# Kernel optimization log

Hardware: AMD Instinct MI355X
Metric: run time of the kernel (lower is better)

Reference implementation:

```python
import jax, jax.numpy as jnp
import numpy as np

B, N, D, H, ADIM = 2048, 8, 128, 512, 6  # batch, n_slots, slot_dim, latent_dim, action_dim
EPS = 1e-5

# static fully-connected edge list (no self-loops), C-SWM convention: row=source (also receiver)
_adj = np.ones((N, N)) - np.eye(N)
_ROW, _COL = np.nonzero(_adj)
ROW = jnp.asarray(_ROW)
COL = jnp.asarray(_COL)
E = N * (N - 1)


def _layernorm(x, g, b):
    m = jnp.mean(x, axis=-1, keepdims=True)
    v = jnp.var(x, axis=-1, keepdims=True)
    return (x - m) * jax.lax.rsqrt(v + EPS) * g + b


def setup_inputs() -> dict:
    key = jax.random.key(0)
    ks = jax.random.split(key, 16)
    s = 0.02
    inp = {
        "slots": jax.random.normal(ks[0], (B, N, D), dtype=jnp.float32),
        # edge MLP: Linear(2D,H) ReLU Linear(H,H) LN ReLU Linear(H,H)
        "ew1": jax.random.normal(ks[1], (H, 2 * D), dtype=jnp.float32) * s,
        "eb1": jnp.zeros((H,), jnp.float32),
        "ew2": jax.random.normal(ks[2], (H, H), dtype=jnp.float32) * s,
        "eb2": jnp.zeros((H,), jnp.float32),
        "eln_g": jnp.ones((H,), jnp.float32),
        "eln_b": jnp.zeros((H,), jnp.float32),
        "ew3": jax.random.normal(ks[3], (H, H), dtype=jnp.float32) * s,
        "eb3": jnp.zeros((H,), jnp.float32),
        # node MLP: Linear(D+H,H) ReLU Linear(H,H) LN ReLU Linear(H,D)
        "nw1": jax.random.normal(ks[4], (H, D + H), dtype=jnp.float32) * s,
        "nb1": jnp.zeros((H,), jnp.float32),
        "nw2": jax.random.normal(ks[5], (H, H), dtype=jnp.float32) * s,
        "nb2": jnp.zeros((H,), jnp.float32),
        "nln_g": jnp.ones((H,), jnp.float32),
        "nln_b": jnp.zeros((H,), jnp.float32),
        "nw3": jax.random.normal(ks[6], (D, H), dtype=jnp.float32) * s,
        "nb3": jnp.zeros((D,), jnp.float32),
        # policy head: Linear(D, 2*action_dim)
        "head_w": jax.random.normal(ks[7], (2 * ADIM, D), dtype=jnp.float32) * s,
        "head_b": jnp.zeros((2 * ADIM,), jnp.float32),
    }
    return inp


def reference(slots, ew1, eb1, ew2, eb2, eln_g, eln_b, ew3, eb3,
              nw1, nb1, nw2, nb2, nln_g, nln_b, nw3, nb3, head_w, head_b):
    # ---- GNN edge model over all ordered pairs (i != j) ----
    src = slots[:, ROW]          # [B, E, D]
    tgt = slots[:, COL]          # [B, E, D]
    e = jnp.concatenate([src, tgt], axis=-1)            # [B, E, 2D]
    e = jax.nn.relu(jnp.einsum('bed,hd->beh', e, ew1) + eb1)
    e = jnp.einsum('beh,gh->beg', e, ew2) + eb2
    e = jax.nn.relu(_layernorm(e, eln_g, eln_b))
    e = jnp.einsum('beh,gh->beg', e, ew3) + eb3         # [B, E, H]
    # scatter-sum messages to source node index (unsorted_segment_sum over ROW)
    agg = jnp.zeros((slots.shape[0], N, e.shape[-1]), e.dtype).at[:, ROW].add(e)
    # ---- node model ----
    x = jnp.concatenate([slots, agg], axis=-1)          # [B, N, D+H]
    x = jax.nn.relu(jnp.einsum('bnd,hd->bnh', x, nw1) + nb1)
    x = jnp.einsum('bnh,gh->bng', x, nw2) + nb2
    x = jax.nn.relu(_layernorm(x, nln_g, nln_b))
    x = jnp.einsum('bnh,dh->bnd', x, nw3) + nb3         # [B, N, D]
    # ---- OCPolicy: ReLU, sum-pool over slots, linear head ----
    x = jax.nn.relu(x)
    pooled = x.sum(axis=1)                              # [B, D]
    return pooled @ head_w.T + head_b                   # [B, 2*ADIM]
```

## Files before the change

### kernel.cpp

```cpp
#include <hip/hip_runtime.h>
#include <cstdint>
#include <cstddef>

typedef _Float16 f16;
typedef _Float16 f16x8 __attribute__((ext_vector_type(8)));
typedef _Float16 f16x4 __attribute__((ext_vector_type(4)));
typedef float f32x4 __attribute__((ext_vector_type(4)));

#define AS1 __attribute__((address_space(1)))
#define AS3 __attribute__((address_space(3)))

__device__ __forceinline__ void gl_lds16(const void* g, void* l) {
    __builtin_amdgcn_global_load_lds((const AS1 uint32_t*)g, (AS3 uint32_t*)l, 16, 0, 0);
}

__device__ __forceinline__ f16x8 relu8(f16x8 x) {
    f16x8 z = {};
    return __builtin_elementwise_max(x, z);
}


__global__ __launch_bounds__(256, 2)
void edge_gemm_fused(const f16* __restrict__ PQ, const f16* __restrict__ W,
                     const float* __restrict__ bias, f16* __restrict__ C)
{
    __shared__ f16 Bs[2][8192];
    __shared__ f16 PQl[2][2048];
    const int tid  = threadIdx.x;
    const int wave = tid >> 6, lane = tid & 63;
    const int wm = wave >> 1, wn = wave & 1;
    const int lr = lane & 15, lk = lane >> 4;
    const int row0 = blockIdx.y << 7;
    const int col0 = blockIdx.x << 8;

    const int sc16 = (((tid & 3) ^ ((tid >> 3) & 3)) << 3);
    const f16* Wg = W + (size_t)(col0 + (tid >> 2)) * 512 + sc16;
    const int b0 = row0 / 56;
    const int n0 = b0 << 3;
    const f16* PQg = PQ + (size_t)(n0 + ((tid & 127) >> 2)) * 1024
                   + ((tid >> 7) << 9) + sc16;

    int addrP[4], addrQ[4];
#pragma unroll
    for (int i = 0; i < 4; ++i) {
        int row = wm * 64 + i * 16 + lr;
        int er  = row0 + row;
        int bb  = er / 56;
        int e   = er - bb * 56;
        int r   = e / 7;
        int t2  = e - r * 7;
        int cn  = t2 + (t2 >= r ? 1 : 0);
        int pr  = ((bb - b0) << 3) + r;
        int qr  = ((bb - b0) << 3) + cn;
        addrP[i] = pr * 32 + ((lk ^ ((pr >> 1) & 3)) << 3);
        addrQ[i] = 1024 + qr * 32 + ((lk ^ ((qr >> 1) & 3)) << 3);
    }
    const int kx = (lk ^ ((lr >> 1) & 3)) << 3;

    f32x4 acc[4][8] = {};

#define STAGE(buf, k0)                                                        \
    do {                                                                      \
        gl_lds16(PQg + (k0), &PQl[buf][tid * 8]);                             \
        _Pragma("unroll")                                                     \
        for (int i_ = 0; i_ < 4; ++i_)                                        \
            gl_lds16(Wg + (k0) + (size_t)(i_ * 64) * 512,                     \
                     &Bs[buf][(i_ * 256 + tid) * 8]);                         \
    } while (0)

    STAGE(0, 0);
    for (int t = 0; t < 16; ++t) {
        const int cur = t & 1;
        if (t < 15) {
            STAGE(cur ^ 1, (t + 1) << 5);
            asm volatile("s_waitcnt vmcnt(5)" ::: "memory");
        } else {
            asm volatile("s_waitcnt vmcnt(0)" ::: "memory");
        }
        __builtin_amdgcn_s_barrier();
        __builtin_amdgcn_sched_barrier(0);

        f16x8 af[4], bf[8];
#pragma unroll
        for (int i = 0; i < 4; ++i) {
            f16x8 p = *(const f16x8*)&PQl[cur][addrP[i]];
            f16x8 q = *(const f16x8*)&PQl[cur][addrQ[i]];
            af[i] = relu8(p + q);
        }
#pragma unroll
        for (int i = 0; i < 8; ++i)
            bf[i] = *(const f16x8*)&Bs[cur][(wn * 128 + i * 16 + lr) * 32 + kx];
#pragma unroll
        for (int mi = 0; mi < 4; ++mi)
#pragma unroll
            for (int ni = 0; ni < 8; ++ni)
                acc[mi][ni] = __builtin_amdgcn_mfma_f32_16x16x32_f16(
                    af[mi], bf[ni], acc[mi][ni], 0, 0, 0);

        __builtin_amdgcn_sched_barrier(0);
        __builtin_amdgcn_s_barrier();
    }
#undef STAGE

#pragma unroll
    for (int mi = 0; mi < 4; ++mi) {
#pragma unroll
        for (int ni = 0; ni < 8; ++ni) {
#pragma unroll
            for (int j = 0; j < 4; ++j) {
                int r = row0 + wm * 64 + mi * 16 + lk * 4 + j;
                int c = col0 + wn * 128 + ni * 16 + lr;
                C[(size_t)r * 512 + c] = (f16)(acc[mi][ni][j] + bias[c]);
            }
        }
    }
}

template<bool RELU>
__global__ __launch_bounds__(256, 2)
void gemm_swz_kernel(const f16* __restrict__ A, int lda,
                     const f16* __restrict__ W, int ldw,
                     const float* __restrict__ bias, float bscale,
                     f16* __restrict__ C, int ldc, int K)
{
    __shared__ f16 As[2][4096];
    __shared__ f16 Bs[2][8192];
    const int tid  = threadIdx.x;
    const int wave = tid >> 6, lane = tid & 63;
    const int wm = wave >> 1, wn = wave & 1;
    const int lr = lane & 15, lk = lane >> 4;
    const int row0 = blockIdx.y << 7;
    const int col0 = blockIdx.x << 8;

    const int c16 = (((tid & 3) ^ ((tid >> 3) & 3)) << 3);
    const f16* Ag = A + (size_t)(row0 + (tid >> 2)) * lda + c16;
    const f16* Wg = W + (size_t)(col0 + (tid >> 2)) * ldw + c16;
    const int kx = (lk ^ ((lr >> 1) & 3)) << 3;

    f32x4 acc[4][8] = {};

#define STAGE(buf, k0)                                                        \
    do {                                                                      \
        gl_lds16(Ag + (k0),                      &As[buf][tid * 8]);          \
        gl_lds16(Ag + (k0) + (size_t)64 * lda,   &As[buf][(tid + 256) * 8]);  \
        _Pragma("unroll")                                                     \
        for (int i_ = 0; i_ < 4; ++i_)                                        \
            gl_lds16(Wg + (k0) + (size_t)(i_ * 64) * ldw,                     \
                     &Bs[buf][(i_ * 256 + tid) * 8]);                         \
    } while (0)

    const int nt = K >> 5;
    STAGE(0, 0);
    for (int t = 0; t < nt; ++t) {
        const int cur = t & 1;
        if (t + 1 < nt) {
            STAGE(cur ^ 1, (t + 1) << 5);
            asm volatile("s_waitcnt vmcnt(6)" ::: "memory");
        } else {
            asm volatile("s_waitcnt vmcnt(0)" ::: "memory");
        }
        __builtin_amdgcn_s_barrier();
        __builtin_amdgcn_sched_barrier(0);

        f16x8 af[4], bf[8];
#pragma unroll
        for (int i = 0; i < 4; ++i)
            af[i] = *(const f16x8*)&As[cur][(wm * 64 + i * 16 + lr) * 32 + kx];
#pragma unroll
        for (int i = 0; i < 8; ++i)
            bf[i] = *(const f16x8*)&Bs[cur][(wn * 128 + i * 16 + lr) * 32 + kx];
#pragma unroll
        for (int mi = 0; mi < 4; ++mi)
#pragma unroll
            for (int ni = 0; ni < 8; ++ni)
                acc[mi][ni] = __builtin_amdgcn_mfma_f32_16x16x32_f16(
                    af[mi], bf[ni], acc[mi][ni], 0, 0, 0);

        __builtin_amdgcn_sched_barrier(0);
        __builtin_amdgcn_s_barrier();
    }
#undef STAGE

#pragma unroll
    for (int mi = 0; mi < 4; ++mi) {
#pragma unroll
        for (int ni = 0; ni < 8; ++ni) {
#pragma unroll
            for (int j = 0; j < 4; ++j) {
                int r = row0 + wm * 64 + mi * 16 + lk * 4 + j;
                int c = col0 + wn * 128 + ni * 16 + lr;
                float v = acc[mi][ni][j] + bias[c] * bscale;
                if (RELU) v = fmaxf(v, 0.0f);
                C[(size_t)r * ldc + c] = (f16)v;
            }
        }
    }
}

template<bool BIAS, bool RELU>
__global__ __launch_bounds__(256, 2)
void gemm_kernel(const f16* __restrict__ A, int lda,
                 const f16* __restrict__ W, int ldw,
                 const float* __restrict__ bias, float bscale,
                 f16* __restrict__ C, int ldc, int K)
{
    __shared__ f16 As[4096];
    __shared__ f16 Bs[4096];
    const int tid  = threadIdx.x;
    const int wave = tid >> 6;
    const int lane = tid & 63;
    const int wm = wave >> 1, wn = wave & 1;
    const int lr = lane & 15, lk = lane >> 4;
    const int row0 = blockIdx.y << 7;
    const int col0 = blockIdx.x << 7;

    const int srow = tid >> 2;
    const int scol = (tid & 3) << 3;
    const f16* Ag = A + (size_t)(row0 + srow) * lda + scol;
    const f16* Wg = W + (size_t)(col0 + srow) * ldw + scol;
    f16* lA0 = &As[wave * 512];
    f16* lA1 = &As[2048 + wave * 512];
    f16* lB0 = &Bs[wave * 512];
    f16* lB1 = &Bs[2048 + wave * 512];

    f32x4 acc[4][4] = {};

    for (int k0 = 0; k0 < K; k0 += 32) {
        if (k0) __syncthreads();
        gl_lds16(Ag + k0,                    lA0);
        gl_lds16(Ag + k0 + (size_t)64 * lda, lA1);
        gl_lds16(Wg + k0,                    lB0);
        gl_lds16(Wg + k0 + (size_t)64 * ldw, lB1);
        __syncthreads();

        f16x8 af[4], bf[4];
#pragma unroll
        for (int i = 0; i < 4; ++i)
            af[i] = *(const f16x8*)&As[(wm * 64 + i * 16 + lr) * 32 + lk * 8];
#pragma unroll
        for (int i = 0; i < 4; ++i)
            bf[i] = *(const f16x8*)&Bs[(wn * 64 + i * 16 + lr) * 32 + lk * 8];
#pragma unroll
        for (int mi = 0; mi < 4; ++mi)
#pragma unroll
            for (int ni = 0; ni < 4; ++ni)
                acc[mi][ni] = __builtin_amdgcn_mfma_f32_16x16x32_f16(
                    af[mi], bf[ni], acc[mi][ni], 0, 0, 0);
    }

#pragma unroll
    for (int mi = 0; mi < 4; ++mi) {
#pragma unroll
        for (int ni = 0; ni < 4; ++ni) {
#pragma unroll
            for (int j = 0; j < 4; ++j) {
                int r = row0 + wm * 64 + mi * 16 + lk * 4 + j;
                int c = col0 + wn * 64 + ni * 16 + lr;
                float v = acc[mi][ni][j];
                if (BIAS) v += bias[c] * bscale;
                if (RELU) v = fmaxf(v, 0.0f);
                C[(size_t)r * ldc + c] = (f16)v;
            }
        }
    }
}

__global__ __launch_bounds__(512, 2)
void fused_gemm_ln(const f16* __restrict__ A, int lda,
                   const f16* __restrict__ W,
                   const float* __restrict__ bias,
                   const float* __restrict__ g, const float* __restrict__ b,
                   f16* __restrict__ C, int ldc)
{
    constexpr int BM = 64, NI = 4, NWN = 8;
    __shared__ f16 As[BM * 32];
    __shared__ f16 Bs[512 * 32];
    __shared__ float lnred[BM * NWN * 2];
    __shared__ float stat[BM * 2];

    const int tid  = threadIdx.x;
    const int wave = tid >> 6;
    const int lane = tid & 63;
    const int wn = wave;
    const int lr = lane & 15, lk = lane >> 4;
    const int row0 = blockIdx.x * BM;
    const int wcol0 = wn * (NI * 16);

    const int c16 = (((tid & 3) ^ ((tid >> 3) & 3)) << 3);
    const f16* Ar = A + (size_t)(row0 + (tid >> 2)) * lda + c16;
    const f16* Wr = W + (size_t)(tid >> 2) * 512 + c16;
    const int kx = (lk ^ ((lr >> 1) & 3)) << 3;

    f32x4 acc[4][NI] = {};

    for (int k0 = 0; k0 < 512; k0 += 32) {
        if (k0) __syncthreads();
#pragma unroll
        for (int i = 0; i < 4; ++i)
            gl_lds16(Wr + k0 + (size_t)(i * 128) * 512, &Bs[(i * 512 + tid) * 8]);
        if (tid < 256)
            gl_lds16(Ar + k0, &As[tid * 8]);
        __syncthreads();

        f16x8 af[4], bf[NI];
#pragma unroll
        for (int i = 0; i < 4; ++i)
            af[i] = *(const f16x8*)&As[(i * 16 + lr) * 32 + kx];
#pragma unroll
        for (int i = 0; i < NI; ++i)
            bf[i] = *(const f16x8*)&Bs[(wcol0 + i * 16 + lr) * 32 + kx];
#pragma unroll
        for (int mi = 0; mi < 4; ++mi)
#pragma unroll
            for (int ni = 0; ni < NI; ++ni)
                acc[mi][ni] = __builtin_amdgcn_mfma_f32_16x16x32_f16(
                    af[mi], bf[ni], acc[mi][ni], 0, 0, 0);
    }

    float biasv[NI], gv[NI], bv[NI];
#pragma unroll
    for (int ni = 0; ni < NI; ++ni) {
        int col = wcol0 + ni * 16 + lr;
        biasv[ni] = bias[col];
        gv[ni] = g[col];
        bv[ni] = b[col];
    }
#pragma unroll
    for (int mi = 0; mi < 4; ++mi)
#pragma unroll
        for (int ni = 0; ni < NI; ++ni)
#pragma unroll
            for (int j = 0; j < 4; ++j)
                acc[mi][ni][j] += biasv[ni];

#pragma unroll
    for (int mi = 0; mi < 4; ++mi) {
#pragma unroll
        for (int j = 0; j < 4; ++j) {
            float s = 0.f, s2 = 0.f;
#pragma unroll
            for (int ni = 0; ni < NI; ++ni) {
                float v = acc[mi][ni][j];
                s += v; s2 += v * v;
            }
#pragma unroll
            for (int o = 1; o < 16; o <<= 1) {
                s  += __shfl_xor(s,  o, 64);
                s2 += __shfl_xor(s2, o, 64);
            }
            if (lr == 0) {
                int row = mi * 16 + lk * 4 + j;
                lnred[(row * NWN + wn) * 2 + 0] = s;
                lnred[(row * NWN + wn) * 2 + 1] = s2;
            }
        }
    }
    __syncthreads();
    if (tid < BM) {
        float s = 0.f, s2 = 0.f;
#pragma unroll
        for (int w = 0; w < NWN; ++w) {
            s  += lnred[(tid * NWN + w) * 2 + 0];
            s2 += lnred[(tid * NWN + w) * 2 + 1];
        }
        float mean = s * (1.0f / 512.0f);
        float var  = fmaxf(s2 * (1.0f / 512.0f) - mean * mean, 0.0f);
        stat[tid * 2 + 0] = mean;
        stat[tid * 2 + 1] = rsqrtf(var + 1e-5f);
    }
    __syncthreads();

#pragma unroll
    for (int mi = 0; mi < 4; ++mi) {
#pragma unroll
        for (int j = 0; j < 4; ++j) {
            int row = mi * 16 + lk * 4 + j;
            float mean = stat[row * 2 + 0];
            float rstd = stat[row * 2 + 1];
            size_t gr = (size_t)(row0 + row) * ldc;
#pragma unroll
            for (int ni = 0; ni < NI; ++ni) {
                float y = (acc[mi][ni][j] - mean) * rstd * gv[ni] + bv[ni];
                C[gr + wcol0 + ni * 16 + lr] = (f16)fmaxf(y, 0.0f);
            }
        }
    }
}

__global__ void convert_all_kernel(
    const float* __restrict__ s0, f16* __restrict__ xcat,
    const float* __restrict__ s1, f16* __restrict__ d1,
    const float* __restrict__ s2, f16* __restrict__ d2,
    const float* __restrict__ s3, f16* __restrict__ d3,
    const float* __restrict__ s4, f16* __restrict__ d4,
    const float* __restrict__ s5, f16* __restrict__ d5,
    const float* __restrict__ s6, f16* __restrict__ d6,
    const float* __restrict__ eb1, float* __restrict__ eb1x)
{
    int q = blockIdx.x * 256 + threadIdx.x;
    if (q >= 852224) return;
    if (q < 524288) {
        const float4 v = *(const float4*)&s0[(size_t)q * 4];
        f16x4 o; o[0]=(f16)v.x; o[1]=(f16)v.y; o[2]=(f16)v.z; o[3]=(f16)v.w;
        int row = q >> 5, col = (q & 31) << 2;
        *(f16x4*)&xcat[(size_t)row * 640 + col] = o;
        return;
    }
    if (q >= 851968) {
        int i = q - 851968;
        int srcq = (i < 128) ? i : i - 128;
        const float4 v = *(const float4*)&eb1[srcq * 4];
        float4 o; o.x = 0.5f*v.x; o.y = 0.5f*v.y; o.z = 0.5f*v.z; o.w = 0.5f*v.w;
        *(float4*)&eb1x[i * 4] = o;
        return;
    }
    if (q < 557056) {
        int i = q - 524288;
        int f = i << 2;
        int n = f >> 8, c = f & 255;
        const float4 v = *(const float4*)&s1[(size_t)f];
        f16x4 o; o[0]=(f16)v.x; o[1]=(f16)v.y; o[2]=(f16)v.z; o[3]=(f16)v.w;
        int dst = (c < 128) ? n * 128 + c : (512 + n) * 128 + (c - 128);
        *(f16x4*)&d1[dst] = o;
        return;
    }
    const float* s; f16* d; int i;
    if      (q < 622592) { s = s2; d = d2; i = q - 557056; }
    else if (q < 688128) { s = s3; d = d3; i = q - 622592; }
    else if (q < 770048) { s = s4; d = d4; i = q - 688128; }
    else if (q < 835584) { s = s5; d = d5; i = q - 770048; }
    else                 { s = s6; d = d6; i = q - 835584; }
    const float4 v = *(const float4*)&s[(size_t)i * 4];
    f16x4 o; o[0]=(f16)v.x; o[1]=(f16)v.y; o[2]=(f16)v.z; o[3]=(f16)v.w;
    *(f16x4*)&d[(size_t)i * 4] = o;
}

__global__ void ln_agg_kernel(const f16* __restrict__ E2,
                              const float* __restrict__ g, const float* __restrict__ b,
                              f16* __restrict__ AGG, int nodes)
{
    int gw   = (blockIdx.x * 256 + threadIdx.x) >> 6;
    int lane = threadIdx.x & 63;
    if (gw >= nodes) return;
    int bb = gw >> 3, n = gw & 7;
    const f16* base = E2 + (((size_t)(bb * 56 + n * 7)) << 9) + (lane << 3);
    f16x8 v[7];
#pragma unroll
    for (int t = 0; t < 7; ++t) v[t] = *(const f16x8*)(base + ((size_t)t << 9));
    float gv[8], bv[8], acc[8] = {};
#pragma unroll
    for (int j = 0; j < 8; ++j) {
        gv[j] = g[(lane << 3) + j];
        bv[j] = b[(lane << 3) + j];
    }
#pragma unroll
    for (int t = 0; t < 7; ++t) {
        float f[8]; float s = 0.f, s2 = 0.f;
#pragma unroll
        for (int j = 0; j < 8; ++j) { f[j] = (float)v[t][j]; s += f[j]; s2 += f[j] * f[j]; }
#pragma unroll
        for (int o = 32; o; o >>= 1) { s += __shfl_xor(s, o, 64); s2 += __shfl_xor(s2, o, 64); }
        float mean = s * (1.0f / 512.0f);
        float var  = fmaxf(s2 * (1.0f / 512.0f) - mean * mean, 0.0f);
        float rstd = rsqrtf(var + 1e-5f);
#pragma unroll
        for (int j = 0; j < 8; ++j)
            acc[j] += fmaxf((f[j] - mean) * rstd * gv[j] + bv[j], 0.0f);
    }
    f16x8 o;
#pragma unroll
    for (int j = 0; j < 8; ++j) o[j] = (f16)acc[j];
    *(f16x8*)&AGG[((size_t)gw << 9) + (lane << 3)] = o;
}

__global__ void head_kernel(const f16* __restrict__ x3, const float* __restrict__ hw,
                            const float* __restrict__ hb, float* __restrict__ out)
{
    __shared__ float pooled[128];
    int b = blockIdx.x, t = threadIdx.x;
    float s = 0.f;
#pragma unroll
    for (int n = 0; n < 8; ++n) s += (float)x3[(((size_t)b * 8 + n) << 7) + t];
    pooled[t] = s;
    __syncthreads();
    if (t < 12) {
        float acc = hb[t];
        for (int d = 0; d < 128; ++d) acc += pooled[d] * hw[t * 128 + d];
        out[b * 12 + t] = acc;
    }
}

extern "C" void kernel_launch(void* const* d_in, const int* in_sizes, int n_in,
                              void* d_out, int out_size, void* d_ws, size_t ws_size,
                              hipStream_t stream)
{
    const float* slots  = (const float*)d_in[0];
    const float* ew1    = (const float*)d_in[1];
    const float* eb1    = (const float*)d_in[2];
    const float* ew2    = (const float*)d_in[3];
    const float* eb2    = (const float*)d_in[4];
    const float* eln_g  = (const float*)d_in[5];
    const float* eln_b  = (const float*)d_in[6];
    const float* ew3    = (const float*)d_in[7];
    const float* eb3    = (const float*)d_in[8];
    const float* nw1    = (const float*)d_in[9];
    const float* nb1    = (const float*)d_in[10];
    const float* nw2    = (const float*)d_in[11];
    const float* nb2    = (const float*)d_in[12];
    const float* nln_g  = (const float*)d_in[13];
    const float* nln_b  = (const float*)d_in[14];
    const float* nw3    = (const float*)d_in[15];
    const float* nb3    = (const float*)d_in[16];
    const float* head_w = (const float*)d_in[17];
    const float* head_b = (const float*)d_in[18];

    char* ws = (char*)d_ws;
    f16*   XCAT    = (f16*)(ws + 0);
    f16*   w_ew1x  = (f16*)(ws + 20971520);
    f16*   w_ew2   = (f16*)(ws + 21233664);
    f16*   w_ew3   = (f16*)(ws + 21757952);
    f16*   w_nw1   = (f16*)(ws + 22282240);
    f16*   w_nw2   = (f16*)(ws + 22937600);
    f16*   w_nw3   = (f16*)(ws + 23461888);
    float* eb1x    = (float*)(ws + 23592960);
    f16*   AGG     = (f16*)(ws + 23597056);
    char*  arena   =        ws + 40374272;

    const size_t FIXED = 40374272ULL;
    int BCH;
    if      (ws_size >= FIXED + 73728ULL * 2048) BCH = 2048;
    else if (ws_size >= FIXED + 73728ULL * 1024) BCH = 1024;
    else                                         BCH = 512;
    const int nch = 2048 / BCH;
    const int RN  = BCH * 8;
    const int RE  = BCH * 56;

    f16* PQc = (f16*)(arena);
    f16* E2c = (f16*)(arena + (size_t)16384 * BCH);

    f16* X1 = AGG;
    f16* X2 = (f16*)(arena);
    f16* X3 = (f16*)(arena + 16777216);
    float* out = (float*)d_out;

    convert_all_kernel<<<dim3(3329), 256, 0, stream>>>(
        slots, XCAT, ew1, w_ew1x, ew2, w_ew2, ew3, w_ew3,
        nw1, w_nw1, nw2, w_nw2, nw3, w_nw3, eb1, eb1x);

    for (int c = 0; c < nch; ++c) {
        const f16* sc = XCAT + (size_t)c * RN * 640;
        gemm_swz_kernel<false><<<dim3(4, RN/128), 256, 0, stream>>>(
            sc, 640, w_ew1x, 128, eb1x, 1.0f, PQc, 1024, 128);
        edge_gemm_fused<<<dim3(2, RE/128), 256, 0, stream>>>(
            PQc, w_ew2, eb2, E2c);
        ln_agg_kernel<<<dim3(RN/4), 256, 0, stream>>>(
            E2c, eln_g, eln_b, AGG + (size_t)c * RN * 512, RN);
    }

    gemm_swz_kernel<false><<<dim3(2,128), 256, 0, stream>>>(
        AGG, 512, w_ew3, 512, eb3, 7.0f, XCAT + 128, 640, 512);
    gemm_swz_kernel<true><<<dim3(2,128), 256, 0, stream>>>(
        XCAT, 640, w_nw1, 640, nb1, 1.0f, X1, 512, 640);
    fused_gemm_ln<<<dim3(256), 512, 0, stream>>>(
        X1, 512, w_nw2, nb2, nln_g, nln_b, X2, 512);
    gemm_kernel<true,true><<<dim3(1,128), 256, 0, stream>>>(
        X2, 512, w_nw3, 512, nb3, 1.0f, X3, 128, 512);

    head_kernel<<<dim3(2048), 128, 0, stream>>>(X3, head_w, head_b, out);
}
```

Before: 220.3 us.

## Fuse edge GEMM with LayerNorm and segment-sum aggregation into one kernel

```diff
diff --git a/kernel.cpp b/kernel.cpp
--- a/kernel.cpp
+++ b/kernel.cpp
@@ -20,80 +20,89 @@
 }
 
 
-__global__ __launch_bounds__(256, 2)
-void edge_gemm_fused(const f16* __restrict__ PQ, const f16* __restrict__ W,
-                     const float* __restrict__ bias, f16* __restrict__ C)
-{
-    __shared__ f16 Bs[2][8192];
-    __shared__ f16 PQl[2][2048];
+__global__ __launch_bounds__(512, 2)
+void edge_ln_agg_kernel(const f16* __restrict__ PQ, const f16* __restrict__ W,
+                        const float* __restrict__ eb2,
+                        const float* __restrict__ g, const float* __restrict__ b,
+                        f16* __restrict__ AGG)
+{
+    __shared__ char smem[77824];
+    f16*   BsB   = (f16*)smem;
+    f16*   PQlB  = (f16*)(smem + 65536);
+    float* lnred = (float*)(smem + 69632);
+    float* stat  = (float*)(smem + 76800);
+
     const int tid  = threadIdx.x;
     const int wave = tid >> 6, lane = tid & 63;
-    const int wm = wave >> 1, wn = wave & 1;
+    const int wn = wave;
     const int lr = lane & 15, lk = lane >> 4;
-    const int row0 = blockIdx.y << 7;
-    const int col0 = blockIdx.x << 8;
-
-    const int sc16 = (((tid & 3) ^ ((tid >> 3) & 3)) << 3);
-    const f16* Wg = W + (size_t)(col0 + (tid >> 2)) * 512 + sc16;
-    const int b0 = row0 / 56;
-    const int n0 = b0 << 3;
-    const f16* PQg = PQ + (size_t)(n0 + ((tid & 127) >> 2)) * 1024
-                   + ((tid >> 7) << 9) + sc16;
-
-    int addrP[4], addrQ[4];
-#pragma unroll
-    for (int i = 0; i < 4; ++i) {
-        int row = wm * 64 + i * 16 + lr;
-        int er  = row0 + row;
-        int bb  = er / 56;
-        int e   = er - bb * 56;
-        int r   = e / 7;
-        int t2  = e - r * 7;
-        int cn  = t2 + (t2 >= r ? 1 : 0);
-        int pr  = ((bb - b0) << 3) + r;
-        int qr  = ((bb - b0) << 3) + cn;
-        addrP[i] = pr * 32 + ((lk ^ ((pr >> 1) & 3)) << 3);
-        addrQ[i] = 1024 + qr * 32 + ((lk ^ ((qr >> 1) & 3)) << 3);
+    const int blk = blockIdx.x;
+    const int row0 = blk * 112;
+    const int n0 = blk << 4;
+
+    const int c16 = (((tid & 3) ^ ((tid >> 3) & 3)) << 3);
+    const f16* Wg = W + (size_t)(tid >> 2) * 512 + c16;
+    const int prow = tid >> 2;
+    const f16* PQg = PQ + (size_t)(n0 + (prow & 15)) * 1024
+                   + ((prow >> 4) << 9) + c16;
+
+    int addrP[7], addrQ[7];
+#pragma unroll
+    for (int mi = 0; mi < 7; ++mi) {
+        int er = row0 + mi * 16 + lr;
+        int bb = er / 56;
+        int e  = er - bb * 56;
+        int r  = e / 7;
+        int t2 = e - r * 7;
+        int cn = t2 + (t2 >= r ? 1 : 0);
+        int pl = ((bb - 2 * blk) << 3) + r;
+        int ql = ((bb - 2 * blk) << 3) + cn;
+        addrP[mi] = pl * 32 + ((lk ^ ((pl >> 1) & 3)) << 3);
+        addrQ[mi] = 512 + ql * 32 + ((lk ^ ((ql >> 1) & 3)) << 3);
     }
     const int kx = (lk ^ ((lr >> 1) & 3)) << 3;
 
-    f32x4 acc[4][8] = {};
+    f32x4 acc[7][4] = {};
 
 #define STAGE(buf, k0)                                                        \
     do {                                                                      \
-        gl_lds16(PQg + (k0), &PQl[buf][tid * 8]);                             \
         _Pragma("unroll")                                                     \
         for (int i_ = 0; i_ < 4; ++i_)                                        \
-            gl_lds16(Wg + (k0) + (size_t)(i_ * 64) * 512,                     \
-                     &Bs[buf][(i_ * 256 + tid) * 8]);                         \
+            gl_lds16(Wg + (k0) + (size_t)(i_ * 128) * 512,                    \
+                     &BsB[(size_t)(buf) * 16384 + (i_ * 512 + tid) * 8]);     \
+        if (tid < 128)                                                        \
+            gl_lds16(PQg + (k0), &PQlB[(size_t)(buf) * 1024 + tid * 8]);      \
     } while (0)
 
     STAGE(0, 0);
     for (int t = 0; t < 16; ++t) {
         const int cur = t & 1;
-        if (t < 15) {
+        if (t + 1 < 16) {
             STAGE(cur ^ 1, (t + 1) << 5);
-            asm volatile("s_waitcnt vmcnt(5)" ::: "memory");
+            if (wave < 2) asm volatile("s_waitcnt vmcnt(5)" ::: "memory");
+            else          asm volatile("s_waitcnt vmcnt(4)" ::: "memory");
         } else {
             asm volatile("s_waitcnt vmcnt(0)" ::: "memory");
         }
         __builtin_amdgcn_s_barrier();
         __builtin_amdgcn_sched_barrier(0);
 
-        f16x8 af[4], bf[8];
-#pragma unroll
-        for (int i = 0; i < 4; ++i) {
-            f16x8 p = *(const f16x8*)&PQl[cur][addrP[i]];
-            f16x8 q = *(const f16x8*)&PQl[cur][addrQ[i]];
-            af[i] = relu8(p + q);
-        }
-#pragma unroll
-        for (int i = 0; i < 8; ++i)
-            bf[i] = *(const f16x8*)&Bs[cur][(wn * 128 + i * 16 + lr) * 32 + kx];
-#pragma unroll
-        for (int mi = 0; mi < 4; ++mi)
-#pragma unroll
-            for (int ni = 0; ni < 8; ++ni)
+        const f16* Pc = &PQlB[(size_t)cur * 1024];
+        const f16* Bc = &BsB[(size_t)cur * 16384];
+        f16x8 af[7], bf[4];
+#pragma unroll
+        for (int mi = 0; mi < 7; ++mi) {
+            f16x8 p = *(const f16x8*)&Pc[addrP[mi]];
+            f16x8 q = *(const f16x8*)&Pc[addrQ[mi]];
+            af[mi] = relu8(p + q);
+        }
+#pragma unroll
+        for (int ni = 0; ni < 4; ++ni)
+            bf[ni] = *(const f16x8*)&Bc[(wn * 64 + ni * 16 + lr) * 32 + kx];
+#pragma unroll
+        for (int mi = 0; mi < 7; ++mi)
+#pragma unroll
+            for (int ni = 0; ni < 4; ++ni)
                 acc[mi][ni] = __builtin_amdgcn_mfma_f32_16x16x32_f16(
                     af[mi], bf[ni], acc[mi][ni], 0, 0, 0);
 
@@ -102,18 +111,84 @@
     }
 #undef STAGE
 
-#pragma unroll
-    for (int mi = 0; mi < 4; ++mi) {
-#pragma unroll
-        for (int ni = 0; ni < 8; ++ni) {
-#pragma unroll
-            for (int j = 0; j < 4; ++j) {
-                int r = row0 + wm * 64 + mi * 16 + lk * 4 + j;
-                int c = col0 + wn * 128 + ni * 16 + lr;
-                C[(size_t)r * 512 + c] = (f16)(acc[mi][ni][j] + bias[c]);
-            }
-        }
-    }
+    float eb2v[4], gv[4], bv[4];
+#pragma unroll
+    for (int ni = 0; ni < 4; ++ni) {
+        int col = wn * 64 + ni * 16 + lr;
+        eb2v[ni] = eb2[col]; gv[ni] = g[col]; bv[ni] = b[col];
+    }
+#pragma unroll
+    for (int mi = 0; mi < 7; ++mi)
+#pragma unroll
+        for (int ni = 0; ni < 4; ++ni)
+#pragma unroll
+            for (int j = 0; j < 4; ++j)
+                acc[mi][ni][j] += eb2v[ni];
+
+#pragma unroll
+    for (int mi = 0; mi < 7; ++mi) {
+#pragma unroll
+        for (int j = 0; j < 4; ++j) {
+            float s = 0.f, s2 = 0.f;
+#pragma unroll
+            for (int ni = 0; ni < 4; ++ni) {
+                float v = acc[mi][ni][j];
+                s += v; s2 += v * v;
+            }
+#pragma unroll
+            for (int o = 1; o < 16; o <<= 1) {
+                s  += __shfl_xor(s,  o, 64);
+                s2 += __shfl_xor(s2, o, 64);
+            }
+            if (lr == 0) {
+                int row = mi * 16 + lk * 4 + j;
+                lnred[(row * 8 + wn) * 2 + 0] = s;
+                lnred[(row * 8 + wn) * 2 + 1] = s2;
+            }
+        }
+    }
+    __syncthreads();
+    if (tid < 112) {
+        float s = 0.f, s2 = 0.f;
+#pragma unroll
+        for (int w = 0; w < 8; ++w) {
+            s  += lnred[(tid * 8 + w) * 2 + 0];
+            s2 += lnred[(tid * 8 + w) * 2 + 1];
+        }
+        float mean = s * (1.0f / 512.0f);
+        float var  = fmaxf(s2 * (1.0f / 512.0f) - mean * mean, 0.0f);
+        stat[tid * 2 + 0] = mean;
+        stat[tid * 2 + 1] = rsqrtf(var + 1e-5f);
+    }
+    __syncthreads();
+
+    float* aggw = (float*)smem + wave * 1024;
+#pragma unroll
+    for (int i = 0; i < 16; ++i) aggw[i * 64 + lane] = 0.f;
+    asm volatile("s_waitcnt lgkmcnt(0)" ::: "memory");
+    for (int turn = 0; turn < 4; ++turn) {
+        if (lk == turn) {
+#pragma unroll
+            for (int mi = 0; mi < 7; ++mi) {
+#pragma unroll
+                for (int j = 0; j < 4; ++j) {
+                    int row = mi * 16 + lk * 4 + j;
+                    float mean = stat[row * 2 + 0];
+                    float rstd = stat[row * 2 + 1];
+                    int gg = row / 7;
+#pragma unroll
+                    for (int ni = 0; ni < 4; ++ni) {
+                        float y = fmaxf((acc[mi][ni][j] - mean) * rstd * gv[ni] + bv[ni], 0.f);
+                        aggw[gg * 64 + ni * 16 + lr] += y;
+                    }
+                }
+            }
+        }
+    }
+    asm volatile("s_waitcnt lgkmcnt(0)" ::: "memory");
+#pragma unroll
+    for (int i = 0; i < 16; ++i)
+        AGG[(size_t)(n0 + i) * 512 + wn * 64 + lane] = (f16)aggw[i * 64 + lane];
 }
 
 template<bool RELU>
@@ -433,44 +508,6 @@
     const float4 v = *(const float4*)&s[(size_t)i * 4];
     f16x4 o; o[0]=(f16)v.x; o[1]=(f16)v.y; o[2]=(f16)v.z; o[3]=(f16)v.w;
     *(f16x4*)&d[(size_t)i * 4] = o;
-}
-
-__global__ void ln_agg_kernel(const f16* __restrict__ E2,
-                              const float* __restrict__ g, const float* __restrict__ b,
-                              f16* __restrict__ AGG, int nodes)
-{
-    int gw   = (blockIdx.x * 256 + threadIdx.x) >> 6;
-    int lane = threadIdx.x & 63;
-    if (gw >= nodes) return;
-    int bb = gw >> 3, n = gw & 7;
-    const f16* base = E2 + (((size_t)(bb * 56 + n * 7)) << 9) + (lane << 3);
-    f16x8 v[7];
-#pragma unroll
-    for (int t = 0; t < 7; ++t) v[t] = *(const f16x8*)(base + ((size_t)t << 9));
-    float gv[8], bv[8], acc[8] = {};
-#pragma unroll
-    for (int j = 0; j < 8; ++j) {
-        gv[j] = g[(lane << 3) + j];
-        bv[j] = b[(lane << 3) + j];
-    }
-#pragma unroll
-    for (int t = 0; t < 7; ++t) {
-        float f[8]; float s = 0.f, s2 = 0.f;
-#pragma unroll
-        for (int j = 0; j < 8; ++j) { f[j] = (float)v[t][j]; s += f[j]; s2 += f[j] * f[j]; }
-#pragma unroll
-        for (int o = 32; o; o >>= 1) { s += __shfl_xor(s, o, 64); s2 += __shfl_xor(s2, o, 64); }
-        float mean = s * (1.0f / 512.0f);
-        float var  = fmaxf(s2 * (1.0f / 512.0f) - mean * mean, 0.0f);
-        float rstd = rsqrtf(var + 1e-5f);
-#pragma unroll
-        for (int j = 0; j < 8; ++j)
-            acc[j] += fmaxf((f[j] - mean) * rstd * gv[j] + bv[j], 0.0f);
-    }
-    f16x8 o;
-#pragma unroll
-    for (int j = 0; j < 8; ++j) o[j] = (f16)acc[j];
-    *(f16x8*)&AGG[((size_t)gw << 9) + (lane << 3)] = o;
 }
 
 __global__ void head_kernel(const f16* __restrict__ x3, const float* __restrict__ hw,
@@ -526,44 +563,29 @@
     f16*   AGG     = (f16*)(ws + 23597056);
     char*  arena   =        ws + 40374272;
 
-    const size_t FIXED = 40374272ULL;
-    int BCH;
-    if      (ws_size >= FIXED + 73728ULL * 2048) BCH = 2048;
-    else if (ws_size >= FIXED + 73728ULL * 1024) BCH = 1024;
-    else                                         BCH = 512;
-    const int nch = 2048 / BCH;
-    const int RN  = BCH * 8;
-    const int RE  = BCH * 56;
-
     f16* PQc = (f16*)(arena);
-    f16* E2c = (f16*)(arena + (size_t)16384 * BCH);
-
-    f16* X1 = AGG;
-    f16* X2 = (f16*)(arena);
-    f16* X3 = (f16*)(arena + 16777216);
+    f16* X1  = AGG;
+    f16* X2  = (f16*)(arena);
+    f16* X3  = (f16*)(arena + 16777216);
     float* out = (float*)d_out;
 
     convert_all_kernel<<<dim3(3329), 256, 0, stream>>>(
         slots, XCAT, ew1, w_ew1x, ew2, w_ew2, ew3, w_ew3,
         nw1, w_nw1, nw2, w_nw2, nw3, w_nw3, eb1, eb1x);
 
-    for (int c = 0; c < nch; ++c) {
-        const f16* sc = XCAT + (size_t)c * RN * 640;
-        gemm_swz_kernel<false><<<dim3(4, RN/128), 256, 0, stream>>>(
-            sc, 640, w_ew1x, 128, eb1x, 1.0f, PQc, 1024, 128);
-        edge_gemm_fused<<<dim3(2, RE/128), 256, 0, stream>>>(
-            PQc, w_ew2, eb2, E2c);
-        ln_agg_kernel<<<dim3(RN/4), 256, 0, stream>>>(
-            E2c, eln_g, eln_b, AGG + (size_t)c * RN * 512, RN);
-    }
-
-    gemm_swz_kernel<false><<<dim3(2,128), 256, 0, stream>>>(
+    gemm_swz_kernel<false><<<dim3(4, 128), 256, 0, stream>>>(
+        XCAT, 640, w_ew1x, 128, eb1x, 1.0f, PQc, 1024, 128);
+
+    edge_ln_agg_kernel<<<dim3(1024), 512, 0, stream>>>(
+        PQc, w_ew2, eb2, eln_g, eln_b, AGG);
+
+    gemm_swz_kernel<false><<<dim3(2, 128), 256, 0, stream>>>(
         AGG, 512, w_ew3, 512, eb3, 7.0f, XCAT + 128, 640, 512);
-    gemm_swz_kernel<true><<<dim3(2,128), 256, 0, stream>>>(
+    gemm_swz_kernel<true><<<dim3(2, 128), 256, 0, stream>>>(
         XCAT, 640, w_nw1, 640, nb1, 1.0f, X1, 512, 640);
     fused_gemm_ln<<<dim3(256), 512, 0, stream>>>(
         X1, 512, w_nw2, nb2, nln_g, nln_b, X2, 512);
-    gemm_kernel<true,true><<<dim3(1,128), 256, 0, stream>>>(
+    gemm_kernel<true,true><<<dim3(1, 128), 256, 0, stream>>>(
         X2, 512, w_nw3, 512, nb3, 1.0f, X3, 128, 512);
 
     head_kernel<<<dim3(2048), 128, 0, stream>>>(X3, head_w, head_b, out);
```

Result: slower. 247.6 us (+12.4%).
